# Kernel tuning notes

Measured on AMD Instinct MI355X. Metric: run time of the kernel, lower is better.

The kernel has to match this reference:

```python
import jax, jax.numpy as jnp
import numpy as np

RES = 14          # window resolution -> N = RES*RES = 196
NUM_HEADS = 24
HEAD_DIM = 32
DIM = NUM_HEADS * HEAD_DIM  # 768
CPB_HIDDEN = 512
BATCH = 128


def _swin2_table_index(res):
    """Swin-v2 continuous relative position bias: log-spaced coords table
    [(2r-1)^2, 2] and relative position index [N*N] (numpy, static)."""
    r = res
    coords = np.arange(-(r - 1), r, dtype=np.float32)
    table = np.stack(np.meshgrid(coords, coords, indexing="ij"), axis=-1)  # [2r-1, 2r-1, 2]
    table = table / (r - 1)  # pretrained_window_size == window_size
    table = table * 8.0
    table = np.sign(table) * np.log2(np.abs(table) + 1.0) / np.log2(8.0)
    table = table.reshape(-1, 2)

    grid = np.stack(np.meshgrid(np.arange(r), np.arange(r), indexing="ij"))  # [2, r, r]
    grid = grid.reshape(2, -1)  # [2, N]
    rel = grid[:, :, None] - grid[:, None, :]  # [2, N, N]
    rel = rel.transpose(1, 2, 0).astype(np.int64)  # [N, N, 2]
    rel[..., 0] += r - 1
    rel[..., 1] += r - 1
    rel[..., 0] *= 2 * r - 1
    index = rel.sum(-1).reshape(-1)  # [N*N]
    return table, index


def setup_inputs() -> dict:
    key = jax.random.key(0)
    ks = jax.random.split(key, 5)
    N = RES * RES
    x = jax.random.normal(ks[0], (BATCH, N, DIM), dtype=jnp.float32)
    qkv_w = jax.random.normal(ks[1], (DIM, 3 * DIM), dtype=jnp.float32) * (DIM ** -0.5)
    qkv_b = jnp.zeros((3 * DIM,), dtype=jnp.float32)
    proj_w = jax.random.normal(ks[2], (DIM, DIM), dtype=jnp.float32) * (DIM ** -0.5)
    proj_b = jnp.zeros((DIM,), dtype=jnp.float32)
    cpb_w1 = jax.random.normal(ks[3], (2, CPB_HIDDEN), dtype=jnp.float32) * (2 ** -0.5)
    cpb_b1 = jnp.zeros((CPB_HIDDEN,), dtype=jnp.float32)
    cpb_w2 = jax.random.normal(ks[4], (CPB_HIDDEN, NUM_HEADS), dtype=jnp.float32) * (CPB_HIDDEN ** -0.5)
    cpb_b2 = jnp.zeros((NUM_HEADS,), dtype=jnp.float32)
    return {"x": x, "qkv_w": qkv_w, "qkv_b": qkv_b, "proj_w": proj_w,
            "proj_b": proj_b, "cpb_w1": cpb_w1, "cpb_b1": cpb_b1,
            "cpb_w2": cpb_w2, "cpb_b2": cpb_b2}


def reference(x, qkv_w, qkv_b, proj_w, proj_b, cpb_w1, cpb_b1, cpb_w2, cpb_b2):
    B, N, C = x.shape
    H, hd = NUM_HEADS, HEAD_DIM

    table_np, index_np = _swin2_table_index(RES)
    table = jnp.asarray(table_np)            # [(2r-1)^2, 2]
    index = jnp.asarray(index_np)            # [N*N] int

    # qkv projection -> (3, B, H, N, hd)
    qkv = x @ qkv_w + qkv_b
    qkv = qkv.reshape(B, N, 3, H, hd).transpose(2, 0, 3, 1, 4)
    q, k, v = qkv[0], qkv[1], qkv[2]

    # scaled QK^T
    attn = jnp.einsum("bhnd,bhmd->bhnm", q, k) / jnp.sqrt(jnp.float32(hd))

    # continuous relative position bias: MLP(2->512->H), gather, 16*sigmoid
    h1 = jax.nn.relu(table @ cpb_w1 + cpb_b1)           # [(2r-1)^2, 512]
    bias_table = h1 @ cpb_w2 + cpb_b2                    # [(2r-1)^2, H]
    bias = bias_table[index].reshape(N, N, H).transpose(2, 0, 1)  # [H, N, N]
    bias = 16.0 * jax.nn.sigmoid(bias)

    attn = jax.nn.softmax(attn + bias[None], axis=-1)

    out = jnp.einsum("bhnm,bhmd->bhnd", attn, v)
    out = out.transpose(0, 2, 1, 3).reshape(B, N, C)
    out = out @ proj_w + proj_b
    return out
```

## Files before the change

kernel.cpp:

```cpp
#include <hip/hip_runtime.h>
#include <hip/hip_bf16.h>

typedef unsigned short u16;
typedef __attribute__((ext_vector_type(8))) short short8;
typedef __attribute__((ext_vector_type(4))) short short4v;
typedef __attribute__((ext_vector_type(8))) u16 u16x8;
typedef __attribute__((ext_vector_type(4))) u16 u16x4;
typedef __attribute__((ext_vector_type(4))) float f32x4;

__device__ __forceinline__ u16 f2bf(float f) {
  __hip_bfloat16 h = __float2bfloat16(f);
  u16 u;
  __builtin_memcpy(&u, &h, 2);
  return u;
}

__device__ __forceinline__ f32x4 mfma16(short8 a, short8 b, f32x4 c) {
  return __builtin_amdgcn_mfma_f32_16x16x32_bf16(a, b, c, 0, 0, 0);
}

__device__ __forceinline__ f32x4 mfma16x16(short4v a, short4v b, f32x4 c) {
#if __has_builtin(__builtin_amdgcn_mfma_f32_16x16x16bf16_1k)
  return __builtin_amdgcn_mfma_f32_16x16x16bf16_1k(a, b, c, 0, 0, 0);
#else
  asm("v_mfma_f32_16x16x16_bf16 %0, %1, %2, %0" : "+v"(c) : "v"(a), "v"(b));
  return c;
#endif
}

__device__ __forceinline__ void gl_lds16(const void* g, void* l) {
  __builtin_amdgcn_global_load_lds(
      (const __attribute__((address_space(1))) unsigned int*)g,
      (__attribute__((address_space(3))) unsigned int*)l, 16, 0, 0);
}

__global__ __launch_bounds__(256) void cvt_x_k(const float* __restrict__ x,
                                               u16* __restrict__ xb) {
  int i = (blockIdx.x * 256 + threadIdx.x) * 4;
  float4 v = *(const float4*)(x + i);
  u16x4 o = { f2bf(v.x), f2bf(v.y), f2bf(v.z), f2bf(v.w) };
  *(u16x4*)(xb + i) = o;
}

__global__ __launch_bounds__(256) void cvt_wt_k(const float* __restrict__ w,
                                                u16* __restrict__ wt, int N) {
  int i = blockIdx.x * 256 + threadIdx.x;
  int nn = i / 768, kk = i % 768;
  wt[i] = f2bf(w[(size_t)kk * N + nn]);
}

__device__ __forceinline__ float cpb_coord(int v) {
  float c = (float)(v - 13) * (8.0f / 13.0f);
  float a = fabsf(c);
  float r = log2f(a + 1.0f) * (1.0f / 3.0f);
  return c < 0.f ? -r : r;
}

__global__ __launch_bounds__(64) void bias_mlp_k(
    const float* __restrict__ w1, const float* __restrict__ b1,
    const float* __restrict__ w2, const float* __restrict__ b2,
    float* __restrict__ btab) {
  int e = blockIdx.x;
  int lane = threadIdx.x;
  float t0 = cpb_coord(e / 27), t1 = cpb_coord(e % 27);
  float acc[24];
#pragma unroll
  for (int hh = 0; hh < 24; hh++) acc[hh] = 0.f;
#pragma unroll
  for (int jj = 0; jj < 8; jj++) {
    int j = lane * 8 + jj;
    float h1 = t0 * w1[j] + t1 * w1[512 + j] + b1[j];
    h1 = fmaxf(h1, 0.f);
#pragma unroll
    for (int hh = 0; hh < 24; hh++) acc[hh] += h1 * w2[j * 24 + hh];
  }
#pragma unroll
  for (int hh = 0; hh < 24; hh++)
#pragma unroll
    for (int m = 1; m < 64; m <<= 1) acc[hh] += __shfl_xor(acc[hh], m, 64);
  if (lane == 0) {
#pragma unroll
    for (int hh = 0; hh < 24; hh++) {
      float v = acc[hh] + b2[hh];
      btab[e * 24 + hh] = 16.f / (1.f + __expf(-v));
    }
  }
}

__global__ __launch_bounds__(256) void bias_expand_k(const float* __restrict__ tab,
                                                     float* __restrict__ be) {
  int i = blockIdx.x * 256 + threadIdx.x;
  int h = i / (196 * 208);
  int rem = i % (196 * 208);
  int row = rem / 208, col = rem % 208;
  float v = 0.f;
  if (col < 196) {
    int dy = row / 14 - col / 14 + 13;
    int dx = row % 14 - col % 14 + 13;
    v = tab[(dy * 27 + dx) * 24 + h] * 1.4426950408889634f;
  }
  be[i] = v;
}

__global__ __launch_bounds__(512) void gemm256_k(
    const u16* __restrict__ A, const u16* __restrict__ Bt,
    const float* __restrict__ bias, u16* __restrict__ Cb, int N, int nbx) {
  __shared__ u16 lds[65536];
  char* ldsb = (char*)lds;
  const int tid = threadIdx.x, lane = tid & 63, w = tid >> 6;
  const int r16 = lane & 15, q4 = lane >> 4;
  const int wm = w >> 2, wn = w & 3;
  const int nwg = gridDim.x;
  const int qq = nwg >> 3, rr = nwg & 7;
  const int xcd = blockIdx.x & 7, bidx = blockIdx.x >> 3;
  const int swz = (xcd < rr) ? xcd * (qq + 1) + bidx
                             : rr * (qq + 1) + (xcd - rr) * qq + bidx;
  const int m0 = (swz / nbx) * 256, n0 = (swz % nbx) * 256;
  const u16* Ab = A + (size_t)m0 * 768;
  const u16* Bb = Bt + (size_t)n0 * 768;

  auto stage = [&](const u16* __restrict__ src, int matBase, int sdst, int h) {
    char* base = ldsb + matBase + (sdst & 1) * 32768 + h * 16384 + w * 1024;
    const int k0 = sdst * 64;
#pragma unroll
    for (int g = 0; g < 2; g++) {
      int c = g * 512 + tid;
      int row = c >> 3, p = c & 7;
      int gch = p ^ (row & 7);
      gl_lds16(src + (size_t)(h * 128 + row) * 768 + k0 + gch * 8,
               base + g * 8192 + lane * 16);
    }
  };

  f32x4 acc[8][4] = {};

  stage(Ab, 0, 0, 0);
  stage(Ab, 0, 0, 1);
  stage(Bb, 65536, 0, 0);
  stage(Bb, 65536, 0, 1);
  stage(Ab, 0, 1, 0);
  asm volatile("s_waitcnt vmcnt(2)" ::: "memory");
  __builtin_amdgcn_s_barrier();

  const int pcb = r16 & 7;
  for (int s = 0; s < 12; s++) {
    const int bA = (s & 1) * 32768;
    const int bB = 65536 + (s & 1) * 32768;
    short8 afr[4][2], bfr[4][2];
#pragma unroll
    for (int i = 0; i < 4; i++)
#pragma unroll
      for (int kk = 0; kk < 2; kk++)
        afr[i][kk] = *(const short8*)(ldsb + bA +
                         (wm * 128 + i * 16 + r16) * 128 +
                         (((kk * 4 + q4) ^ pcb) << 4));
#pragma unroll
    for (int j = 0; j < 4; j++)
#pragma unroll
      for (int kk = 0; kk < 2; kk++)
        bfr[j][kk] = *(const short8*)(ldsb + bB +
                         (wn * 64 + j * 16 + r16) * 128 +
                         (((kk * 4 + q4) ^ pcb) << 4));
    if (s < 11) stage(Ab, 0, s + 1, 1);
    __builtin_amdgcn_s_barrier();
    __builtin_amdgcn_s_setprio(1);
#pragma unroll
    for (int kk = 0; kk < 2; kk++)
#pragma unroll
      for (int i = 0; i < 4; i++)
#pragma unroll
        for (int j = 0; j < 2; j++)
          acc[i][j] = mfma16(afr[i][kk], bfr[j][kk], acc[i][j]);
    __builtin_amdgcn_s_setprio(0);
    __builtin_amdgcn_s_barrier();
    if (s < 11) stage(Bb, 65536, s + 1, 0);
    __builtin_amdgcn_s_barrier();
    __builtin_amdgcn_s_setprio(1);
#pragma unroll
    for (int kk = 0; kk < 2; kk++)
#pragma unroll
      for (int i = 0; i < 4; i++)
#pragma unroll
        for (int j = 2; j < 4; j++)
          acc[i][j] = mfma16(afr[i][kk], bfr[j][kk], acc[i][j]);
    __builtin_amdgcn_s_setprio(0);
    __builtin_amdgcn_s_barrier();
#pragma unroll
    for (int i = 0; i < 4; i++)
#pragma unroll
      for (int kk = 0; kk < 2; kk++)
        afr[i][kk] = *(const short8*)(ldsb + bA +
                         (wm * 128 + (4 + i) * 16 + r16) * 128 +
                         (((kk * 4 + q4) ^ pcb) << 4));
    if (s < 11) stage(Bb, 65536, s + 1, 1);
    __builtin_amdgcn_s_barrier();
    __builtin_amdgcn_s_setprio(1);
#pragma unroll
    for (int kk = 0; kk < 2; kk++)
#pragma unroll
      for (int i = 0; i < 4; i++)
#pragma unroll
        for (int j = 0; j < 2; j++)
          acc[4 + i][j] = mfma16(afr[i][kk], bfr[j][kk], acc[4 + i][j]);
    __builtin_amdgcn_s_setprio(0);
    __builtin_amdgcn_s_barrier();
    if (s < 10) {
      stage(Ab, 0, s + 2, 0);
      asm volatile("s_waitcnt vmcnt(2)" ::: "memory");
    } else if (s == 10) {
      asm volatile("s_waitcnt vmcnt(0)" ::: "memory");
    }
    __builtin_amdgcn_s_barrier();
    __builtin_amdgcn_s_setprio(1);
#pragma unroll
    for (int kk = 0; kk < 2; kk++)
#pragma unroll
      for (int i = 0; i < 4; i++)
#pragma unroll
        for (int j = 2; j < 4; j++)
          acc[4 + i][j] = mfma16(afr[i][kk], bfr[j][kk], acc[4 + i][j]);
    __builtin_amdgcn_s_setprio(0);
    __builtin_amdgcn_s_barrier();
  }

  const int nb = n0 + wn * 64 + r16;
  float bn[4];
#pragma unroll
  for (int j = 0; j < 4; j++) bn[j] = bias[nb + j * 16];
#pragma unroll
  for (int mf = 0; mf < 8; mf++) {
#pragma unroll
    for (int r = 0; r < 4; r++) {
      int m = m0 + wm * 128 + mf * 16 + q4 * 4 + r;
      u16* cp = Cb + (size_t)m * N + nb;
#pragma unroll
      for (int j = 0; j < 4; j++) cp[j * 16] = f2bf(acc[mf][j][r] + bn[j]);
    }
  }
}

__global__ __launch_bounds__(256) void gemm_k(
    const u16* __restrict__ A, const u16* __restrict__ Bt,
    const float* __restrict__ bias, float* __restrict__ Cf,
    int N, int K, int nbx) {
  __shared__ u16 As[128 * 64];
  __shared__ u16 Bs[128 * 64];
  const int tid = threadIdx.x, lane = tid & 63, w = tid >> 6;
  const int r16 = lane & 15, q4 = lane >> 4;
  const int wr = w >> 1, wc = w & 1;
  const int nwg = gridDim.x, cpx = nwg >> 3;
  const int swz = (blockIdx.x & 7) * cpx + (blockIdx.x >> 3);
  const int m0 = (swz / nbx) * 128, n0 = (swz % nbx) * 128;

  f32x4 acc[4][4] = {};

  for (int k0 = 0; k0 < K; k0 += 64) {
#pragma unroll
    for (int g = 0; g < 4; g++) {
      int chunk = (w * 4 + g) * 64 + lane;
      int row = chunk >> 3, p = chunk & 7;
      int gch = p ^ (row & 7);
      gl_lds16(A + (size_t)(m0 + row) * K + k0 + gch * 8, (char*)As + (w * 4 + g) * 1024);
      gl_lds16(Bt + (size_t)(n0 + row) * K + k0 + gch * 8, (char*)Bs + (w * 4 + g) * 1024);
    }
    __syncthreads();
#pragma unroll
    for (int kk = 0; kk < 2; kk++) {
      short8 af[4], bfr[4];
#pragma unroll
      for (int i = 0; i < 4; i++) {
        int row = wr * 64 + i * 16 + r16;
        int pc = (kk * 4 + q4) ^ (r16 & 7);
        af[i] = *(const short8*)((const char*)As + row * 128 + pc * 16);
      }
#pragma unroll
      for (int j = 0; j < 4; j++) {
        int row = wc * 64 + j * 16 + r16;
        int pc = (kk * 4 + q4) ^ (r16 & 7);
        bfr[j] = *(const short8*)((const char*)Bs + row * 128 + pc * 16);
      }
#pragma unroll
      for (int i = 0; i < 4; i++)
#pragma unroll
        for (int j = 0; j < 4; j++) acc[i][j] = mfma16(af[i], bfr[j], acc[i][j]);
    }
    __syncthreads();
  }

  const int nb = n0 + wc * 64 + r16;
  float bn[4];
#pragma unroll
  for (int j = 0; j < 4; j++) bn[j] = bias[nb + j * 16];
#pragma unroll
  for (int i = 0; i < 4; i++) {
#pragma unroll
    for (int r = 0; r < 4; r++) {
      int m = m0 + wr * 64 + i * 16 + q4 * 4 + r;
      float* cp = Cf + (size_t)m * N + nb;
#pragma unroll
      for (int j = 0; j < 4; j++) cp[j * 16] = acc[i][j][r] + bn[j];
    }
  }
}

__global__ __launch_bounds__(256) void attn_k(
    const u16* __restrict__ qkv, const float* __restrict__ be,
    u16* __restrict__ ao) {
  constexpr int VST = 236;
  __shared__ u16 Ks[208 * 32];
  __shared__ u16 Vt[32 * VST];
  const int tid = threadIdx.x, lane = tid & 63, w = tid >> 6;
  const int r16 = lane & 15, q4 = lane >> 4;
  const int bh = blockIdx.x, b = bh / 24, h = bh % 24;
  const u16* qp = qkv + (size_t)(b * 196) * 2304 + h * 32;
  const u16* kp = qp + 768;
  const u16* vp = qp + 1536;
  const float* bp = be + h * (196 * 208);
  const int ksw = (q4 ^ ((r16 >> 1) & 3)) * 16;
  const float SC2 = 0.17677669529663687f * 1.4426950408889634f;

  for (int g = w; g < 13; g += 4) {
    int chunk = g * 64 + lane;
    int row = chunk >> 2;
    int gch = (chunk & 3) ^ ((row >> 1) & 3);
    gl_lds16(kp + (size_t)row * 2304 + gch * 8, (char*)Ks + g * 1024);
  }
  for (int c = tid; c < 784; c += 256) {
    int n = c >> 2, d0 = (c & 3) * 8;
    u16x8 vv = *(const u16x8*)(vp + (size_t)n * 2304 + (c & 3) * 8);
#pragma unroll
    for (int jj = 0; jj < 8; jj++) Vt[(d0 + jj) * VST + n] = vv[jj];
  }
  for (int idx = tid; idx < 32 * 40; idx += 256) {
    int d = idx / 40, n = 196 + idx % 40;
    Vt[d * VST + n] = 0;
  }
  __syncthreads();

  const f32x4 z = {0.f, 0.f, 0.f, 0.f};
  short8 bq = *(const short8*)(qp + (size_t)(w * 16 + r16) * 2304 + q4 * 8);
  for (int si = w; si < 13; si += 4) {
    short8 bq_next = {};
    if (si + 4 < 13)
      bq_next = *(const short8*)(qp + (size_t)((si + 4) * 16 + r16) * 2304 + q4 * 8);
    int gc = si * 16 + r16;
    gc = gc < 196 ? gc : 195;
    const float* brow = bp + gc * 208 + q4 * 4;
    float s0 = 0.f, s1 = 0.f, s2 = 0.f, s3 = 0.f;
    short4v pa[13];
#pragma unroll
    for (int t = 0; t < 13; t++) {
      short8 ka = *(const short8*)((const char*)Ks + (t * 16 + r16) * 64 + ksw);
      f32x4 p = mfma16(ka, bq, z);
      float4 bv = *(const float4*)(brow + t * 16);
      float e0 = __builtin_amdgcn_exp2f(p[0] * SC2 + bv.x);
      float e1 = __builtin_amdgcn_exp2f(p[1] * SC2 + bv.y);
      float e2 = __builtin_amdgcn_exp2f(p[2] * SC2 + bv.z);
      float e3 = __builtin_amdgcn_exp2f(p[3] * SC2 + bv.w);
      if (t == 12) {
        int k0 = 192 + q4 * 4;
        e0 = (k0 + 0 < 196) ? e0 : 0.f;
        e1 = (k0 + 1 < 196) ? e1 : 0.f;
        e2 = (k0 + 2 < 196) ? e2 : 0.f;
        e3 = (k0 + 3 < 196) ? e3 : 0.f;
      }
      s0 += e0; s1 += e1; s2 += e2; s3 += e3;
      pa[t][0] = (short)f2bf(e0);
      pa[t][1] = (short)f2bf(e1);
      pa[t][2] = (short)f2bf(e2);
      pa[t][3] = (short)f2bf(e3);
    }
    bq = bq_next;
    float sum = (s0 + s1) + (s2 + s3);
    sum += __shfl_xor(sum, 16, 64);
    sum += __shfl_xor(sum, 32, 64);
    float rs = 1.0f / sum;
    f32x4 o0a = z, o0b = z, o1a = z, o1b = z;
    __builtin_amdgcn_s_setprio(1);
#pragma unroll
    for (int t = 0; t < 13; t++) {
      const u16* vrow = &Vt[r16 * VST + t * 16 + q4 * 4];
      short4v b0 = *(const short4v*)vrow;
      short4v b1 = *(const short4v*)(vrow + 16 * VST);
      if (t & 1) {
        o0b = mfma16x16(pa[t], b0, o0b);
        o1b = mfma16x16(pa[t], b1, o1b);
      } else {
        o0a = mfma16x16(pa[t], b0, o0a);
        o1a = mfma16x16(pa[t], b1, o1a);
      }
    }
    __builtin_amdgcn_s_setprio(0);
#pragma unroll
    for (int r = 0; r < 4; r++) {
      float rsv = __shfl(rs, q4 * 4 + r, 16);
      int grow = si * 16 + q4 * 4 + r;
      if (grow < 196) {
        u16* op = ao + ((size_t)(b * 196 + grow)) * 768 + h * 32;
        op[r16] = f2bf((o0a[r] + o0b[r]) * rsv);
        op[16 + r16] = f2bf((o1a[r] + o1b[r]) * rsv);
      }
    }
  }
}

extern "C" void kernel_launch(void* const* d_in, const int* in_sizes, int n_in,
                              void* d_out, int out_size, void* d_ws, size_t ws_size,
                              hipStream_t stream) {
  const float* x = (const float*)d_in[0];
  const float* qkv_w = (const float*)d_in[1];
  const float* qkv_b = (const float*)d_in[2];
  const float* proj_w = (const float*)d_in[3];
  const float* proj_b = (const float*)d_in[4];
  const float* cpb_w1 = (const float*)d_in[5];
  const float* cpb_b1 = (const float*)d_in[6];
  const float* cpb_w2 = (const float*)d_in[7];
  const float* cpb_b2 = (const float*)d_in[8];
  float* out = (float*)d_out;

  char* ws = (char*)d_ws;
  size_t o = 0;
  auto alloc = [&](size_t sz) {
    size_t r = o;
    o = (o + sz + 255) & ~(size_t)255;
    return r;
  };
  const size_t ME = (size_t)25088 * 768;
  u16* x_bf = (u16*)(ws + alloc(ME * 2));
  u16* wq_t = (u16*)(ws + alloc((size_t)2304 * 768 * 2));
  u16* wp_t = (u16*)(ws + alloc((size_t)768 * 768 * 2));
  u16* qkv_s = (u16*)(ws + alloc(3 * ME * 2));
  float* btab = (float*)(ws + alloc((size_t)729 * 24 * 4));
  float* bexp = (float*)(ws + alloc((size_t)24 * 196 * 208 * 4));
  u16* ao = x_bf;

  cvt_x_k<<<18816, 256, 0, stream>>>(x, x_bf);
  cvt_wt_k<<<6912, 256, 0, stream>>>(qkv_w, wq_t, 2304);
  cvt_wt_k<<<2304, 256, 0, stream>>>(proj_w, wp_t, 768);
  bias_mlp_k<<<729, 64, 0, stream>>>(cpb_w1, cpb_b1, cpb_w2, cpb_b2, btab);
  bias_expand_k<<<3822, 256, 0, stream>>>(btab, bexp);
  gemm256_k<<<882, 512, 0, stream>>>(x_bf, wq_t, qkv_b, qkv_s, 2304, 9);
  attn_k<<<3072, 256, 0, stream>>>(qkv_s, bexp, ao);
  gemm_k<<<1176, 256, 0, stream>>>(ao, wp_t, proj_b, out, 768, 768, 6);
}
```

Measured before the change: 283.9 us.

## Deepen QKV GEMM prefetch to two steps and tile the weight transpose

```diff
diff --git a/kernel.cpp b/kernel.cpp
--- a/kernel.cpp
+++ b/kernel.cpp
@@ -44,9 +44,20 @@
 
 __global__ __launch_bounds__(256) void cvt_wt_k(const float* __restrict__ w,
                                                 u16* __restrict__ wt, int N) {
-  int i = blockIdx.x * 256 + threadIdx.x;
-  int nn = i / 768, kk = i % 768;
-  wt[i] = f2bf(w[(size_t)kk * N + nn]);
+  __shared__ u16 t64[64][65];
+  const int n0 = blockIdx.x * 64, k0 = blockIdx.y * 64;
+  const int c = threadIdx.x & 63, rg = threadIdx.x >> 6;
+#pragma unroll
+  for (int r = 0; r < 16; r++) {
+    int kk = rg * 16 + r;
+    t64[c][kk] = f2bf(w[(size_t)(k0 + kk) * N + n0 + c]);
+  }
+  __syncthreads();
+#pragma unroll
+  for (int r = 0; r < 16; r++) {
+    int nn = rg * 16 + r;
+    wt[(size_t)(n0 + nn) * 768 + k0 + c] = t64[nn][c];
+  }
 }
 
 __device__ __forceinline__ float cpb_coord(int v) {
@@ -139,13 +150,17 @@
   stage(Bb, 65536, 0, 0);
   stage(Bb, 65536, 0, 1);
   stage(Ab, 0, 1, 0);
-  asm volatile("s_waitcnt vmcnt(2)" ::: "memory");
+  stage(Ab, 0, 1, 1);
+  stage(Bb, 65536, 1, 0);
+  stage(Bb, 65536, 1, 1);
+  asm volatile("s_waitcnt vmcnt(8)" ::: "memory");
   __builtin_amdgcn_s_barrier();
 
   const int pcb = r16 & 7;
   for (int s = 0; s < 12; s++) {
     const int bA = (s & 1) * 32768;
     const int bB = 65536 + (s & 1) * 32768;
+    const bool pf = (s < 10);
     short8 afr[4][2], bfr[4][2];
 #pragma unroll
     for (int i = 0; i < 4; i++)
@@ -161,7 +176,6 @@
         bfr[j][kk] = *(const short8*)(ldsb + bB +
                          (wn * 64 + j * 16 + r16) * 128 +
                          (((kk * 4 + q4) ^ pcb) << 4));
-    if (s < 11) stage(Ab, 0, s + 1, 1);
     __builtin_amdgcn_s_barrier();
     __builtin_amdgcn_s_setprio(1);
 #pragma unroll
@@ -173,7 +187,7 @@
           acc[i][j] = mfma16(afr[i][kk], bfr[j][kk], acc[i][j]);
     __builtin_amdgcn_s_setprio(0);
     __builtin_amdgcn_s_barrier();
-    if (s < 11) stage(Bb, 65536, s + 1, 0);
+    if (pf) stage(Bb, 65536, s + 2, 0);
     __builtin_amdgcn_s_barrier();
     __builtin_amdgcn_s_setprio(1);
 #pragma unroll
@@ -192,7 +206,7 @@
         afr[i][kk] = *(const short8*)(ldsb + bA +
                          (wm * 128 + (4 + i) * 16 + r16) * 128 +
                          (((kk * 4 + q4) ^ pcb) << 4));
-    if (s < 11) stage(Bb, 65536, s + 1, 1);
+    if (pf) stage(Bb, 65536, s + 2, 1);
     __builtin_amdgcn_s_barrier();
     __builtin_amdgcn_s_setprio(1);
 #pragma unroll
@@ -204,9 +218,10 @@
           acc[4 + i][j] = mfma16(afr[i][kk], bfr[j][kk], acc[4 + i][j]);
     __builtin_amdgcn_s_setprio(0);
     __builtin_amdgcn_s_barrier();
-    if (s < 10) {
+    if (pf) {
       stage(Ab, 0, s + 2, 0);
-      asm volatile("s_waitcnt vmcnt(2)" ::: "memory");
+      stage(Ab, 0, s + 2, 1);
+      asm volatile("s_waitcnt vmcnt(8)" ::: "memory");
     } else if (s == 10) {
       asm volatile("s_waitcnt vmcnt(0)" ::: "memory");
     }
@@ -435,8 +450,8 @@
   u16* ao = x_bf;
 
   cvt_x_k<<<18816, 256, 0, stream>>>(x, x_bf);
-  cvt_wt_k<<<6912, 256, 0, stream>>>(qkv_w, wq_t, 2304);
-  cvt_wt_k<<<2304, 256, 0, stream>>>(proj_w, wp_t, 768);
+  cvt_wt_k<<<dim3(36, 12), 256, 0, stream>>>(qkv_w, wq_t, 2304);
+  cvt_wt_k<<<dim3(12, 12), 256, 0, stream>>>(proj_w, wp_t, 768);
   bias_mlp_k<<<729, 64, 0, stream>>>(cpb_w1, cpb_b1, cpb_w2, cpb_b2, btab);
   bias_expand_k<<<3822, 256, 0, stream>>>(btab, bexp);
   gemm256_k<<<882, 512, 0, stream>>>(x_bf, wq_t, qkv_b, qkv_s, 2304, 9);
```

Result: faster. 272.9 us (-3.9%).
